# Optimization experiments

Measured on AMD Instinct MI355X. Metric: run time of the kernel, lower is better.

## Reference

```python
import jax, jax.numpy as jnp
import numpy as np

P = 0.1  # channel error probability (init kwarg error_prob)


def _binary_entropy(p):
    # matches tensor_binary_entropy: clamp log2 at dtype min
    q = 1.0 - p
    min_real = jnp.finfo(jnp.float32).min
    l2p = jnp.maximum(jnp.log2(p), min_real)
    l2q = jnp.maximum(jnp.log2(q), min_real)
    return -p * l2p - q * l2q


def setup_inputs() -> dict:
    key = jax.random.key(0)
    k1, k2, k3, k4 = jax.random.split(key, 4)
    B, L, V = 128, 64, 4096
    logits = jax.random.normal(k1, (B, L, V), jnp.float32)
    probs = jax.nn.softmax(logits, axis=-1)          # relaxed one-hot probs
    entropy = jax.random.uniform(k2, (B, L), jnp.float32)
    rand_mask = jax.random.uniform(k3, (B, L), jnp.float32)
    replacement_ids = jax.random.randint(k4, (B, L), 0, V - 2)
    return {"probs": probs, "entropy": entropy,
            "rand_mask": rand_mask, "replacement_ids": replacement_ids}


def reference(probs, entropy, rand_mask, replacement_ids):
    # SymmetricChannel.gs, training branch, fully vectorized / predicated.
    B, L, V = probs.shape
    mask = rand_mask < P                                  # [B,L] target positions
    any_hit = mask.any()                                  # torch early-returns if sum()==0

    # torch: replaced_probs[:, replacement_symbols] = 1 - eos  -> every masked row
    # is written at EVERY column appearing among the masked replacement ids.
    col_hit = jnp.zeros((V,), bool).at[replacement_ids.reshape(-1)].max(mask.reshape(-1))

    eos = probs[..., :1]                                  # [B,L,1] original EOS prob
    col = jnp.arange(V)
    base = jnp.where(col == 0, eos, jnp.zeros_like(eos))  # replaced_probs[:,0]=eos
    replaced = jnp.where(col_hit, 1.0 - eos, base)        # [B,L,V]

    probs_out = jnp.where(mask[..., None] & any_hit, replaced, probs)

    # torch adds H_b(p) + log2(probs.size(1) - 2)  (size(1) == max_len, kept faithfully)
    delta = _binary_entropy(jnp.float32(P)) + jnp.log2(jnp.float32(L - 2))
    entropy_out = jnp.where(any_hit, entropy + delta, entropy)
    return probs_out, entropy_out
```

## Files before the change

### kernel.cpp

```cpp
#include <hip/hip_runtime.h>


#define V_DIM   4096
#define N_ROWS  8192
#define P_CONST 0.1f
#define DELTA_CONST 6.4231919039761563f

__global__ __launch_bounds__(1024)
void sc_colhit_kernel(const float* __restrict__ rand_mask,
                      const int*   __restrict__ repl,
                      const float* __restrict__ entropy,
                      unsigned*    __restrict__ colhit_out,
                      float*       __restrict__ entropy_out)
{
    __shared__ unsigned colhit[V_DIM / 32];
    __shared__ unsigned anyhit;
    const int t = threadIdx.x;
    if (t < V_DIM / 32) colhit[t] = 0u;
    if (t == 0) anyhit = 0u;
    __syncthreads();

    bool local_any = false;
    #pragma unroll
    for (int k = 0; k < N_ROWS / 1024; ++k) {
        const int i = t + k * 1024;
        if (rand_mask[i] < P_CONST) {
            const int id = repl[i];
            atomicOr(&colhit[id >> 5], 1u << (id & 31));
            local_any = true;
        }
    }
    if (local_any) atomicOr(&anyhit, 1u);
    __syncthreads();

    if (t < V_DIM / 32) colhit_out[t] = colhit[t];
    const float d = anyhit ? DELTA_CONST : 0.0f;
    #pragma unroll
    for (int k = 0; k < N_ROWS / 1024; ++k) {
        const int i = t + k * 1024;
        entropy_out[i] = entropy[i] + d;
    }
}

__global__ __launch_bounds__(256)
void sc_probs_kernel(const float4*   __restrict__ probs4,
                     const float*    __restrict__ probs_s,
                     const float*    __restrict__ rand_mask,
                     const unsigned* __restrict__ colhit_g,
                     float4*         __restrict__ out4)
{
    __shared__ unsigned colhit[V_DIM / 32];
    const int row = blockIdx.x;
    const int t   = threadIdx.x;

    if (t < V_DIM / 32) colhit[t] = colhit_g[t];
    __syncthreads();

    const bool m = rand_mask[row] < P_CONST;
    const long rowbase4 = (long)row * (V_DIM / 4);

    if (m) {
        const float eos = probs_s[(long)row * V_DIM];
        const float om  = 1.0f - eos;
        #pragma unroll
        for (int k = 0; k < 4; ++k) {
            const int c4 = t + k * 256;
            const unsigned w = colhit[c4 >> 3];
            const int c0 = c4 * 4;
            float4 r;
            r.x = ((w >> ( c0      & 31)) & 1u) ? om : ((c0 == 0) ? eos : 0.0f);
            r.y = ((w >> ((c0 + 1) & 31)) & 1u) ? om : 0.0f;
            r.z = ((w >> ((c0 + 2) & 31)) & 1u) ? om : 0.0f;
            r.w = ((w >> ((c0 + 3) & 31)) & 1u) ? om : 0.0f;
            out4[rowbase4 + c4] = r;
        }
    } else {
        #pragma unroll
        for (int k = 0; k < 4; ++k) {
            const int c4 = t + k * 256;
            out4[rowbase4 + c4] = probs4[rowbase4 + c4];
        }
    }
}

extern "C" void kernel_launch(void* const* d_in, const int* in_sizes, int n_in,
                              void* d_out, int out_size, void* d_ws, size_t ws_size,
                              hipStream_t stream)
{
    const float* probs       = (const float*)d_in[0];
    const float* entropy     = (const float*)d_in[1];
    const float* rand_mask   = (const float*)d_in[2];
    const int*   repl        = (const int*)  d_in[3];

    float*    out        = (float*)d_out;
    float*    probs_out  = out;
    float*    entropy_out= out + (long)N_ROWS * V_DIM;
    unsigned* colhit_ws  = (unsigned*)d_ws;

    sc_colhit_kernel<<<1, 1024, 0, stream>>>(rand_mask, repl, entropy,
                                             colhit_ws, entropy_out);

    sc_probs_kernel<<<N_ROWS, 256, 0, stream>>>((const float4*)probs, probs,
                                                rand_mask, colhit_ws,
                                                (float4*)probs_out);
}
```

Before: 49.50 us.

## Fuse column-hit and probs kernels, recompute hit bitmap per masked row

Merges the two launches into one grid. Each masked row block rebuilds the column-hit bitmap itself from the full mask and replacement ids, and 32 extra blocks handle the entropy update and any-hit flag. This removes the serial single-block prologue kernel and the launch gap between kernels. In exchange, about 10% of blocks redundantly scan 8192 mask entries with shared atomics. Copies now use nontemporal loads and stores.

```diff
diff --git a/kernel.cpp b/kernel.cpp
--- a/kernel.cpp
+++ b/kernel.cpp
@@ -6,80 +6,81 @@
 #define P_CONST 0.1f
 #define DELTA_CONST 6.4231919039761563f
 
-__global__ __launch_bounds__(1024)
-void sc_colhit_kernel(const float* __restrict__ rand_mask,
-                      const int*   __restrict__ repl,
-                      const float* __restrict__ entropy,
-                      unsigned*    __restrict__ colhit_out,
-                      float*       __restrict__ entropy_out)
+typedef float f32x4 __attribute__((ext_vector_type(4)));
+
+__global__ __launch_bounds__(256)
+void sc_fused_kernel(const f32x4* __restrict__ probs4,
+                     const float* __restrict__ probs_s,
+                     const f32x4* __restrict__ rand4,
+                     const float* __restrict__ rand_s,
+                     const int*   __restrict__ repl,
+                     const float* __restrict__ entropy,
+                     f32x4*       __restrict__ out4,
+                     float*       __restrict__ entropy_out)
 {
     __shared__ unsigned colhit[V_DIM / 32];
-    __shared__ unsigned anyhit;
-    const int t = threadIdx.x;
-    if (t < V_DIM / 32) colhit[t] = 0u;
-    if (t == 0) anyhit = 0u;
-    __syncthreads();
+    __shared__ unsigned anyflag;
+    const int t   = threadIdx.x;
+    const int bid = blockIdx.x;
 
-    bool local_any = false;
-    #pragma unroll
-    for (int k = 0; k < N_ROWS / 1024; ++k) {
-        const int i = t + k * 1024;
-        if (rand_mask[i] < P_CONST) {
-            const int id = repl[i];
-            atomicOr(&colhit[id >> 5], 1u << (id & 31));
-            local_any = true;
-        }
-    }
-    if (local_any) atomicOr(&anyhit, 1u);
-    __syncthreads();
+    if (bid < N_ROWS) {
+        const int  row      = bid;
+        const long rowbase4 = (long)row * (V_DIM / 4);
+        const bool m        = rand_s[row] < P_CONST;
 
-    if (t < V_DIM / 32) colhit_out[t] = colhit[t];
-    const float d = anyhit ? DELTA_CONST : 0.0f;
-    #pragma unroll
-    for (int k = 0; k < N_ROWS / 1024; ++k) {
-        const int i = t + k * 1024;
-        entropy_out[i] = entropy[i] + d;
-    }
-}
+        if (m) {
+            if (t < V_DIM / 32) colhit[t] = 0u;
+            __syncthreads();
+            #pragma unroll
+            for (int k = 0; k < N_ROWS / 4 / 256; ++k) {
+                const int   i4 = t + k * 256;
+                const f32x4 r  = rand4[i4];
+                const int   i0 = i4 * 4;
+                if (r.x < P_CONST) { const int id = repl[i0    ]; atomicOr(&colhit[id >> 5], 1u << (id & 31)); }
+                if (r.y < P_CONST) { const int id = repl[i0 + 1]; atomicOr(&colhit[id >> 5], 1u << (id & 31)); }
+                if (r.z < P_CONST) { const int id = repl[i0 + 2]; atomicOr(&colhit[id >> 5], 1u << (id & 31)); }
+                if (r.w < P_CONST) { const int id = repl[i0 + 3]; atomicOr(&colhit[id >> 5], 1u << (id & 31)); }
+            }
+            __syncthreads();
 
-__global__ __launch_bounds__(256)
-void sc_probs_kernel(const float4*   __restrict__ probs4,
-                     const float*    __restrict__ probs_s,
-                     const float*    __restrict__ rand_mask,
-                     const unsigned* __restrict__ colhit_g,
-                     float4*         __restrict__ out4)
-{
-    __shared__ unsigned colhit[V_DIM / 32];
-    const int row = blockIdx.x;
-    const int t   = threadIdx.x;
-
-    if (t < V_DIM / 32) colhit[t] = colhit_g[t];
-    __syncthreads();
-
-    const bool m = rand_mask[row] < P_CONST;
-    const long rowbase4 = (long)row * (V_DIM / 4);
-
-    if (m) {
-        const float eos = probs_s[(long)row * V_DIM];
-        const float om  = 1.0f - eos;
-        #pragma unroll
-        for (int k = 0; k < 4; ++k) {
-            const int c4 = t + k * 256;
-            const unsigned w = colhit[c4 >> 3];
-            const int c0 = c4 * 4;
-            float4 r;
-            r.x = ((w >> ( c0      & 31)) & 1u) ? om : ((c0 == 0) ? eos : 0.0f);
-            r.y = ((w >> ((c0 + 1) & 31)) & 1u) ? om : 0.0f;
-            r.z = ((w >> ((c0 + 2) & 31)) & 1u) ? om : 0.0f;
-            r.w = ((w >> ((c0 + 3) & 31)) & 1u) ? om : 0.0f;
-            out4[rowbase4 + c4] = r;
+            const float eos = probs_s[(long)row * V_DIM];
+            const float om  = 1.0f - eos;
+            #pragma unroll
+            for (int k = 0; k < 4; ++k) {
+                const int      c4 = t + k * 256;
+                const unsigned w  = colhit[c4 >> 3];
+                const int      c0 = c4 * 4;
+                f32x4 r;
+                r.x = ((w >> ( c0      & 31)) & 1u) ? om : ((c0 == 0) ? eos : 0.0f);
+                r.y = ((w >> ((c0 + 1) & 31)) & 1u) ? om : 0.0f;
+                r.z = ((w >> ((c0 + 2) & 31)) & 1u) ? om : 0.0f;
+                r.w = ((w >> ((c0 + 3) & 31)) & 1u) ? om : 0.0f;
+                __builtin_nontemporal_store(r, &out4[rowbase4 + c4]);
+            }
+        } else {
+            #pragma unroll
+            for (int k = 0; k < 4; ++k) {
+                const int   c4 = t + k * 256;
+                const f32x4 v  = __builtin_nontemporal_load(&probs4[rowbase4 + c4]);
+                __builtin_nontemporal_store(v, &out4[rowbase4 + c4]);
+            }
         }
     } else {
+        const int eb = bid - N_ROWS;
+        if (t == 0) anyflag = 0u;
+        __syncthreads();
+        bool la = false;
         #pragma unroll
-        for (int k = 0; k < 4; ++k) {
-            const int c4 = t + k * 256;
-            out4[rowbase4 + c4] = probs4[rowbase4 + c4];
+        for (int k = 0; k < N_ROWS / 4 / 256; ++k) {
+            const f32x4 r = rand4[t + k * 256];
+            la = la || (r.x < P_CONST) || (r.y < P_CONST) ||
+                       (r.z < P_CONST) || (r.w < P_CONST);
         }
+        if (la) atomicOr(&anyflag, 1u);
+        __syncthreads();
+        const float d = anyflag ? DELTA_CONST : 0.0f;
+        const int   i = eb * 256 + t;
+        entropy_out[i] = entropy[i] + d;
     }
 }
 
@@ -87,20 +88,18 @@
                               void* d_out, int out_size, void* d_ws, size_t ws_size,
                               hipStream_t stream)
 {
-    const float* probs       = (const float*)d_in[0];
-    const float* entropy     = (const float*)d_in[1];
-    const float* rand_mask   = (const float*)d_in[2];
-    const int*   repl        = (const int*)  d_in[3];
+    const float* probs     = (const float*)d_in[0];
+    const float* entropy   = (const float*)d_in[1];
+    const float* rand_mask = (const float*)d_in[2];
+    const int*   repl      = (const int*)  d_in[3];
 
-    float*    out        = (float*)d_out;
-    float*    probs_out  = out;
-    float*    entropy_out= out + (long)N_ROWS * V_DIM;
-    unsigned* colhit_ws  = (unsigned*)d_ws;
+    float* out         = (float*)d_out;
+    float* probs_out   = out;
+    float* entropy_out = out + (long)N_ROWS * V_DIM;
 
-    sc_colhit_kernel<<<1, 1024, 0, stream>>>(rand_mask, repl, entropy,
-                                             colhit_ws, entropy_out);
-
-    sc_probs_kernel<<<N_ROWS, 256, 0, stream>>>((const float4*)probs, probs,
-                                                rand_mask, colhit_ws,
-                                                (float4*)probs_out);
+    sc_fused_kernel<<<N_ROWS + 32, 256, 0, stream>>>(
+        (const f32x4*)probs, probs,
+        (const f32x4*)rand_mask, rand_mask,
+        repl, entropy,
+        (f32x4*)probs_out, entropy_out);
 }
```

Result: no change. 50.39 us (+1.8%).
